# Kernel optimization log

Hardware: AMD Instinct MI355X
Metric: run time of the kernel (lower is better)

Reference implementation:

```python
import jax, jax.numpy as jnp
import numpy as np

LAYER_START = 4   # module init arg layer_start
WIN = 2           # module init arg context_window_size
EPS = 1e-8        # clamp in cosine_similarity_torch


def setup_inputs() -> dict:
    key = jax.random.key(0)
    k1, k2 = jax.random.split(key)
    L_all, B, S, D = 13, 8, 512, 768  # BERT-base: embeddings + 12 layers
    hidden_states = jax.random.normal(k1, (L_all, B, S, D), dtype=jnp.float32)
    lengths = jax.random.randint(k2, (B,), S // 2, S + 1)
    attention_mask = (jnp.arange(S)[None, :] < lengths[:, None]).astype(jnp.int32)
    return {"hidden_states": hidden_states, "attention_mask": attention_mask}


def _wk_forward(hidden_states, attention_mask):
    # hidden_states: (L_all, B, S, D) -> keep layers from LAYER_START on
    x = jnp.transpose(hidden_states, (1, 0, 2, 3))[:, LAYER_START:]  # (B, L, S, D)
    B, L, S, D = x.shape
    feats = jnp.transpose(x, (0, 2, 1, 3))  # (B, S, L, D) per-token layer features

    # ---- unify_token: per-token, QR over windowed layer embeddings ----
    aligns, novs = [], []
    for k in range(L):  # small fixed loop over layers (9 iters)
        left = list(range(k - WIN, k)) if k >= WIN else []
        right = list(range(k + 1, min(k + WIN + 1, L)))
        idx = np.array(left + right + [k])
        n = idx.size  # = window_matrix.size(0) in torch
        A = jnp.swapaxes(feats[:, :, idx, :], -1, -2)  # (B, S, D, n) = window_matrix.T
        _, R = jnp.linalg.qr(A)                        # R: (B, S, n, n)
        r = R[..., :, -1]                              # last column of R
        Rsub = R[..., :-1, :-1]
        # columns of Rsub normalized along dim 0, mean over columns, dot R[:-1,-1]
        Rhat = Rsub / jnp.linalg.norm(Rsub, axis=-2, keepdims=True)
        align = jnp.sum(jnp.mean(Rhat, axis=-1) * R[..., :-1, -1], axis=-1)
        align = align / jnp.linalg.norm(r[..., :-1], axis=-1)
        align = 1.0 / (align * (n * 2))
        nov = jnp.abs(r[..., -1]) / jnp.linalg.norm(r, axis=-1)
        aligns.append(align)
        novs.append(nov)
    align = jnp.stack(aligns, axis=-1)  # (B, S, L)
    nov = jnp.stack(novs, axis=-1)      # (B, S, L)
    align = align / jnp.sum(align, axis=-1, keepdims=True)
    nov = nov / jnp.sum(nov, axis=-1, keepdims=True)
    alpha = align + nov
    alpha = alpha / jnp.sum(alpha, axis=-1, keepdims=True)
    token_emb = jnp.einsum('bsl,bsld->bsd', alpha, feats)  # per-token embedding

    # ---- unify_sentence: variance of sub-diagonal cosine sims across layers ----
    norms = jnp.linalg.norm(feats, axis=-1)  # (B, S, L)
    c = jnp.sum(feats[:, :, 1:] * feats[:, :, :-1], axis=-1)
    c = c / jnp.clip(norms[:, :, 1:] * norms[:, :, :-1], EPS)  # (B, S, L-1)
    var_tok = jnp.var(c, axis=-1, ddof=1)  # torch.var is unbiased

    lengths = jnp.sum(attention_mask, axis=1) - 1  # unmask_num
    valid = jnp.arange(S)[None, :] < lengths[:, None]
    v = jnp.where(valid, var_tok, 0.0)
    v = v / jnp.sum(v, axis=-1, keepdims=True)
    return jnp.einsum('bs,bsd->bd', v, token_emb)  # (B, D)


def reference(hidden_states, attention_mask):
    return _wk_forward(hidden_states, attention_mask)
```

## Files before the change

kernel.cpp:

```cpp
#include <hip/hip_runtime.h>

#define B_ 8
#define S_ 512
#define D_ 768
#define LAYER0 4
#define LSTRIDE4 (8*512*768/4)
#define SCH 32
#define CW (S_/SCH)

__device__ const int QI9[45] = {0,0,0,0,0,0,0,0,0, 1,1,1,1,1,1,1,1, 2,2,2,2,2,2,2,
                                3,3,3,3,3,3, 4,4,4,4,4, 5,5,5,5, 6,6,6, 7,7, 8};
__device__ const int QJ9[45] = {0,1,2,3,4,5,6,7,8, 1,2,3,4,5,6,7,8, 2,3,4,5,6,7,8,
                                3,4,5,6,7,8, 4,5,6,7,8, 5,6,7,8, 6,7,8, 7,8, 8};

__device__ __forceinline__ float dot4(const float4& a, const float4& b) {
  return fmaf(a.x, b.x, fmaf(a.y, b.y, fmaf(a.z, b.z, a.w * b.w)));
}

__global__ __launch_bounds__(64) void wk_token(const float* __restrict__ hid,
                                               const int* __restrict__ mask,
                                               float* __restrict__ wte,
                                               float* __restrict__ wv) {
  const int token = blockIdx.x;
  const int b = token >> 9;
  const int s = token & (S_ - 1);
  const int t = threadIdx.x;

  __shared__ float pgl[64][45];
  __shared__ float Gsym[81];
  __shared__ float st[19];

  const int valid = (s < S_ - 1) ? mask[b * S_ + s + 1] : 0;

  const float4* base = (const float4*)hid
      + (((size_t)LAYER0 * B_ + b) * S_ + s) * (D_ / 4) + t;
  float4 f[27];
#pragma unroll
  for (int l = 0; l < 9; ++l) {
#pragma unroll
    for (int c = 0; c < 3; ++c) f[l * 3 + c] = base[(size_t)l * LSTRIDE4 + c * 64];
  }

  {
    int q = 0;
#pragma unroll
    for (int i = 0; i < 9; ++i) {
#pragma unroll
      for (int j = i; j < 9; ++j) {
        pgl[t][q] = dot4(f[i * 3], f[j * 3])
                  + dot4(f[i * 3 + 1], f[j * 3 + 1])
                  + dot4(f[i * 3 + 2], f[j * 3 + 2]);
        ++q;
      }
    }
  }
  __syncthreads();

  if (t < 45) {
    float a0 = 0.f, a1 = 0.f, a2 = 0.f, a3 = 0.f;
#pragma unroll
    for (int r = 0; r < 64; r += 4) {
      a0 += pgl[r][t]; a1 += pgl[r + 1][t]; a2 += pgl[r + 2][t]; a3 += pgl[r + 3][t];
    }
    float tot = (a0 + a1) + (a2 + a3);
    Gsym[QI9[t] * 9 + QJ9[t]] = tot;
    Gsym[QJ9[t] * 9 + QI9[t]] = tot;
  }
  __syncthreads();

  if (t < 9) {
    const int k = t;
    int nb[4]; int m = 0;
    if (k >= 2) { nb[m++] = k - 2; nb[m++] = k - 1; }
    if (k + 1 < 9) nb[m++] = k + 1;
    if (k + 2 < 9) nb[m++] = k + 2;
    const int n = m + 1;

    float g[4], Lc[4][4], tv[4];
    for (int i = 0; i < m; ++i) g[i] = Gsym[nb[i] * 9 + k];

    for (int i = 0; i < m; ++i) {
      for (int j = 0; j <= i; ++j) {
        float sum = Gsym[nb[i] * 9 + nb[j]];
        for (int p = 0; p < j; ++p) sum -= Lc[i][p] * Lc[j][p];
        Lc[i][j] = (i == j) ? sqrtf(sum) : sum / Lc[j][j];
      }
    }
    float s2 = 0.f;
    for (int i = 0; i < m; ++i) {
      float sum = g[i];
      for (int p = 0; p < i; ++p) sum -= Lc[i][p] * tv[p];
      tv[i] = sum / Lc[i][i];
      s2 += tv[i] * tv[i];
    }
    float ar = 0.f;
    for (int i = 0; i < m; ++i) ar += g[i] / sqrtf(Gsym[nb[i] * 9 + nb[i]]);
    ar /= (float)m;

    st[k] = sqrtf(s2) / (ar * (2.0f * (float)n));
    float Gkk = Gsym[k * 9 + k];
    st[9 + k] = sqrtf(fmaxf(Gkk - s2, 0.f)) / sqrtf(Gkk);
  }
  if (t == 9) {
    float sc = 0.f, sc2 = 0.f;
    for (int i = 0; i < 8; ++i) {
      float nn = sqrtf(Gsym[i * 9 + i]) * sqrtf(Gsym[(i + 1) * 9 + i + 1]);
      nn = fmaxf(nn, 1e-8f);
      float ci = Gsym[i * 9 + i + 1] / nn;
      sc += ci; sc2 += ci * ci;
    }
    float mean = sc * 0.125f;
    st[18] = (sc2 - 8.f * mean * mean) * (1.f / 7.f);
  }
  __syncthreads();

  const float w = valid ? st[18] : 0.f;
  float sa = 0.f, sn = 0.f;
#pragma unroll
  for (int l = 0; l < 9; ++l) { sa += st[l]; sn += st[9 + l]; }
  const float rsa = 1.f / sa, rsn = 1.f / sn;
  float a9[9]; float ss = 0.f;
#pragma unroll
  for (int l = 0; l < 9; ++l) { a9[l] = st[l] * rsa + st[9 + l] * rsn; ss += a9[l]; }
  const float inv = w / ss;

  float4* o = (float4*)wte + (size_t)token * (D_ / 4) + t;
#pragma unroll
  for (int c = 0; c < 3; ++c) {
    float4 acc = make_float4(0.f, 0.f, 0.f, 0.f);
#pragma unroll
    for (int l = 0; l < 9; ++l) {
      float a = a9[l] * inv;
      float4 p = f[l * 3 + c];
      acc.x += a * p.x; acc.y += a * p.y; acc.z += a * p.z; acc.w += a * p.w;
    }
    o[c * 64] = acc;
  }
  if (t == 0) wv[token] = w;
}

__global__ __launch_bounds__(192) void wk_pool(const float* __restrict__ wte,
                                               const float* __restrict__ wv,
                                               float* __restrict__ P,
                                               float* __restrict__ Pw) {
  const int b = blockIdx.x >> 5;
  const int c = blockIdx.x & 31;
  const int t = threadIdx.x;

  float4 a = make_float4(0.f, 0.f, 0.f, 0.f);
  const float4* base = (const float4*)wte + ((size_t)b * S_ + c * CW) * (D_ / 4) + t;
#pragma unroll 4
  for (int sl = 0; sl < CW; ++sl) {
    float4 p = base[sl * (D_ / 4)];
    a.x += p.x; a.y += p.y; a.z += p.z; a.w += p.w;
  }
  ((float4*)P)[(size_t)blockIdx.x * (D_ / 4) + t] = a;
  if (t == 0) {
    float ws = 0.f;
#pragma unroll
    for (int i = 0; i < CW; ++i) ws += wv[b * S_ + c * CW + i];
    Pw[blockIdx.x] = ws;
  }
}

__global__ __launch_bounds__(256) void wk_pool_final(const float* __restrict__ P,
                                                     const float* __restrict__ Pw,
                                                     float* __restrict__ out) {
  const int i = blockIdx.x * 256 + threadIdx.x;
  const int b = i / (D_ / 4);
  const int d4 = i % (D_ / 4);
  float n0 = 0.f, n1 = 0.f, n2 = 0.f, n3 = 0.f, den = 0.f;
#pragma unroll
  for (int c = 0; c < SCH; ++c) {
    float4 p = ((const float4*)P)[((size_t)b * SCH + c) * (D_ / 4) + d4];
    n0 += p.x; n1 += p.y; n2 += p.z; n3 += p.w;
    den += Pw[b * SCH + c];
  }
  float inv = 1.f / den;
  ((float4*)out)[i] = make_float4(n0 * inv, n1 * inv, n2 * inv, n3 * inv);
}

extern "C" void kernel_launch(void* const* d_in, const int* in_sizes, int n_in,
                              void* d_out, int out_size, void* d_ws, size_t ws_size,
                              hipStream_t stream) {
  const float* hid = (const float*)d_in[0];
  const int* mask = (const int*)d_in[1];
  float* out = (float*)d_out;

  float* wte = (float*)d_ws;
  float* wv  = wte + (size_t)B_ * S_ * D_;
  float* P   = wv + B_ * S_;
  float* Pw  = P + (size_t)B_ * SCH * D_;

  wk_token<<<B_ * S_, 64, 0, stream>>>(hid, mask, wte, wv);
  wk_pool<<<B_ * SCH, 192, 0, stream>>>(wte, wv, P, Pw);
  wk_pool_final<<<(B_ * (D_ / 4) + 255) / 256, 256, 0, stream>>>(P, Pw, out);
}
```

Before: 52.29 us.

## Emit per-token layer weights and re-read hidden states in the pooling kernel

The token kernel no longer keeps all nine layers of features in registers. It streams one 256-float chunk at a time into Gram partials and reduces them with wave shuffles before a smaller LDS stage. Instead of writing a 768-wide weighted token embedding, it writes nine per-token layer weights. The pooling kernel then re-reads the nine hidden-state layers and applies those weights itself. This removes the intermediate embedding write and read and lowers register pressure, but the large hidden-state tensor is read twice, and the second read happens in a kernel with only 256 blocks.

```diff
diff --git a/kernel.cpp b/kernel.cpp
--- a/kernel.cpp
+++ b/kernel.cpp
@@ -17,16 +17,15 @@
   return fmaf(a.x, b.x, fmaf(a.y, b.y, fmaf(a.z, b.z, a.w * b.w)));
 }
 
-__global__ __launch_bounds__(64) void wk_token(const float* __restrict__ hid,
-                                               const int* __restrict__ mask,
-                                               float* __restrict__ wte,
-                                               float* __restrict__ wv) {
+__global__ __launch_bounds__(64, 4) void wk_token(const float* __restrict__ hid,
+                                                  const int* __restrict__ mask,
+                                                  float* __restrict__ wa) {
   const int token = blockIdx.x;
   const int b = token >> 9;
   const int s = token & (S_ - 1);
   const int t = threadIdx.x;
 
-  __shared__ float pgl[64][45];
+  __shared__ float pgl[16][45];
   __shared__ float Gsym[81];
   __shared__ float st[19];
 
@@ -34,35 +33,43 @@
 
   const float4* base = (const float4*)hid
       + (((size_t)LAYER0 * B_ + b) * S_ + s) * (D_ / 4) + t;
-  float4 f[27];
-#pragma unroll
-  for (int l = 0; l < 9; ++l) {
-#pragma unroll
-    for (int c = 0; c < 3; ++c) f[l * 3 + c] = base[(size_t)l * LSTRIDE4 + c * 64];
-  }
-
-  {
+  float pp[45];
+#pragma unroll
+  for (int q = 0; q < 45; ++q) pp[q] = 0.f;
+
+#pragma unroll
+  for (int c = 0; c < 3; ++c) {
+    float4 g[9];
+#pragma unroll
+    for (int l = 0; l < 9; ++l) g[l] = base[(size_t)l * LSTRIDE4 + c * 64];
     int q = 0;
 #pragma unroll
     for (int i = 0; i < 9; ++i) {
 #pragma unroll
       for (int j = i; j < 9; ++j) {
-        pgl[t][q] = dot4(f[i * 3], f[j * 3])
-                  + dot4(f[i * 3 + 1], f[j * 3 + 1])
-                  + dot4(f[i * 3 + 2], f[j * 3 + 2]);
+        pp[q] += dot4(g[i], g[j]);
         ++q;
       }
     }
   }
+
+#pragma unroll
+  for (int q = 0; q < 45; ++q) {
+    pp[q] += __shfl_xor(pp[q], 1);
+    pp[q] += __shfl_xor(pp[q], 2);
+  }
+  if ((t & 3) == 0) {
+    const int r = t >> 2;
+#pragma unroll
+    for (int q = 0; q < 45; ++q) pgl[r][q] = pp[q];
+  }
   __syncthreads();
 
   if (t < 45) {
-    float a0 = 0.f, a1 = 0.f, a2 = 0.f, a3 = 0.f;
-#pragma unroll
-    for (int r = 0; r < 64; r += 4) {
-      a0 += pgl[r][t]; a1 += pgl[r + 1][t]; a2 += pgl[r + 2][t]; a3 += pgl[r + 3][t];
-    }
-    float tot = (a0 + a1) + (a2 + a3);
+    float a0 = 0.f, a1 = 0.f;
+#pragma unroll
+    for (int r = 0; r < 16; r += 2) { a0 += pgl[r][t]; a1 += pgl[r + 1][t]; }
+    float tot = a0 + a1;
     Gsym[QI9[t] * 9 + QJ9[t]] = tot;
     Gsym[QJ9[t] * 9 + QI9[t]] = tot;
   }
@@ -114,51 +121,51 @@
   }
   __syncthreads();
 
-  const float w = valid ? st[18] : 0.f;
-  float sa = 0.f, sn = 0.f;
-#pragma unroll
-  for (int l = 0; l < 9; ++l) { sa += st[l]; sn += st[9 + l]; }
-  const float rsa = 1.f / sa, rsn = 1.f / sn;
-  float a9[9]; float ss = 0.f;
-#pragma unroll
-  for (int l = 0; l < 9; ++l) { a9[l] = st[l] * rsa + st[9 + l] * rsn; ss += a9[l]; }
-  const float inv = w / ss;
-
-  float4* o = (float4*)wte + (size_t)token * (D_ / 4) + t;
-#pragma unroll
-  for (int c = 0; c < 3; ++c) {
-    float4 acc = make_float4(0.f, 0.f, 0.f, 0.f);
-#pragma unroll
-    for (int l = 0; l < 9; ++l) {
-      float a = a9[l] * inv;
-      float4 p = f[l * 3 + c];
-      acc.x += a * p.x; acc.y += a * p.y; acc.z += a * p.z; acc.w += a * p.w;
-    }
-    o[c * 64] = acc;
-  }
-  if (t == 0) wv[token] = w;
-}
-
-__global__ __launch_bounds__(192) void wk_pool(const float* __restrict__ wte,
-                                               const float* __restrict__ wv,
+  if (t < 9) {
+    float sa = 0.f, sn = 0.f;
+#pragma unroll
+    for (int l = 0; l < 9; ++l) { sa += st[l]; sn += st[9 + l]; }
+    const float rsa = 1.f / sa, rsn = 1.f / sn;
+    float ss = 0.f;
+#pragma unroll
+    for (int l = 0; l < 9; ++l) ss += st[l] * rsa + st[9 + l] * rsn;
+    const float w = valid ? st[18] : 0.f;
+    const float al = st[t] * rsa + st[9 + t] * rsn;
+    wa[token * 9 + t] = al * (w / ss);
+  }
+}
+
+__global__ __launch_bounds__(192) void wk_pool(const float* __restrict__ hid,
+                                               const float* __restrict__ wa,
                                                float* __restrict__ P,
                                                float* __restrict__ Pw) {
   const int b = blockIdx.x >> 5;
   const int c = blockIdx.x & 31;
   const int t = threadIdx.x;
 
+  __shared__ float ca[CW][9];
+  if (t < CW * 9) ((float*)ca)[t] = wa[((size_t)b * S_ + c * CW) * 9 + t];
+  __syncthreads();
+
   float4 a = make_float4(0.f, 0.f, 0.f, 0.f);
-  const float4* base = (const float4*)wte + ((size_t)b * S_ + c * CW) * (D_ / 4) + t;
+  const float4* base = (const float4*)hid
+      + (((size_t)LAYER0 * B_ + b) * S_ + c * CW) * (D_ / 4) + t;
+#pragma unroll
+  for (int l = 0; l < 9; ++l) {
 #pragma unroll 4
-  for (int sl = 0; sl < CW; ++sl) {
-    float4 p = base[sl * (D_ / 4)];
-    a.x += p.x; a.y += p.y; a.z += p.z; a.w += p.w;
+    for (int sl = 0; sl < CW; ++sl) {
+      float wgt = ca[sl][l];
+      float4 p = base[(size_t)l * LSTRIDE4 + sl * (D_ / 4)];
+      a.x += wgt * p.x; a.y += wgt * p.y; a.z += wgt * p.z; a.w += wgt * p.w;
+    }
   }
   ((float4*)P)[(size_t)blockIdx.x * (D_ / 4) + t] = a;
   if (t == 0) {
     float ws = 0.f;
 #pragma unroll
-    for (int i = 0; i < CW; ++i) ws += wv[b * S_ + c * CW + i];
+    for (int sl = 0; sl < CW; ++sl)
+#pragma unroll
+      for (int l = 0; l < 9; ++l) ws += ca[sl][l];
     Pw[blockIdx.x] = ws;
   }
 }
@@ -187,12 +194,11 @@
   const int* mask = (const int*)d_in[1];
   float* out = (float*)d_out;
 
-  float* wte = (float*)d_ws;
-  float* wv  = wte + (size_t)B_ * S_ * D_;
-  float* P   = wv + B_ * S_;
-  float* Pw  = P + (size_t)B_ * SCH * D_;
-
-  wk_token<<<B_ * S_, 64, 0, stream>>>(hid, mask, wte, wv);
-  wk_pool<<<B_ * SCH, 192, 0, stream>>>(wte, wv, P, Pw);
+  float* wa = (float*)d_ws;
+  float* P  = wa + (size_t)B_ * S_ * 9;
+  float* Pw = P + (size_t)B_ * SCH * D_;
+
+  wk_token<<<B_ * S_, 64, 0, stream>>>(hid, mask, wa);
+  wk_pool<<<B_ * SCH, 192, 0, stream>>>(hid, wa, P, Pw);
   wk_pool_final<<<(B_ * (D_ / 4) + 255) / 256, 256, 0, stream>>>(P, Pw, out);
 }
```

After: 131.3 us. 2.51x slower.

## Fuse token weighting with partial pooling in 4-token blocks, drop intermediate buffer

Applied to the files above, without the earlier changes.

Each block now handles four tokens, one per wavefront, and sums their weighted token embeddings in shared memory before writing one partial row per block. This removes the full per-token embedding write and the separate pooling kernel that read it back, leaving one lighter final reduction kernel. The cost is larger shared memory per block, extra block-wide barriers across the four wavefronts, and a longer final reduction over 128 partials per batch.

```diff
diff --git a/kernel.cpp b/kernel.cpp
--- a/kernel.cpp
+++ b/kernel.cpp
@@ -3,10 +3,10 @@
 #define B_ 8
 #define S_ 512
 #define D_ 768
+#define D4 (D_/4)
 #define LAYER0 4
 #define LSTRIDE4 (8*512*768/4)
-#define SCH 32
-#define CW (S_/SCH)
+#define CPB 128
 
 __device__ const int QI9[45] = {0,0,0,0,0,0,0,0,0, 1,1,1,1,1,1,1,1, 2,2,2,2,2,2,2,
                                 3,3,3,3,3,3, 4,4,4,4,4, 5,5,5,5, 6,6,6, 7,7, 8};
@@ -17,23 +17,25 @@
   return fmaf(a.x, b.x, fmaf(a.y, b.y, fmaf(a.z, b.z, a.w * b.w)));
 }
 
-__global__ __launch_bounds__(64) void wk_token(const float* __restrict__ hid,
-                                               const int* __restrict__ mask,
-                                               float* __restrict__ wte,
-                                               float* __restrict__ wv) {
-  const int token = blockIdx.x;
-  const int b = token >> 9;
-  const int s = token & (S_ - 1);
-  const int t = threadIdx.x;
+__global__ __launch_bounds__(256, 3) void wk_main(const float* __restrict__ hid,
+                                                  const int* __restrict__ mask,
+                                                  float* __restrict__ P,
+                                                  float* __restrict__ Pw) {
+  const int blk = blockIdx.x;
+  const int wid = threadIdx.x >> 6;
+  const int lane = threadIdx.x & 63;
+  const int token = blk * 4 + wid;
+  const int b = token >> 9, s = token & (S_ - 1);
 
-  __shared__ float pgl[64][45];
-  __shared__ float Gsym[81];
-  __shared__ float st[19];
+  __shared__ float pgl[4][64][45];
+  __shared__ float Gsym[4][81];
+  __shared__ float st[4][19];
+  __shared__ float wl[4];
 
   const int valid = (s < S_ - 1) ? mask[b * S_ + s + 1] : 0;
 
   const float4* base = (const float4*)hid
-      + (((size_t)LAYER0 * B_ + b) * S_ + s) * (D_ / 4) + t;
+      + (((size_t)LAYER0 * B_ + b) * S_ + s) * D4 + lane;
   float4 f[27];
 #pragma unroll
   for (int l = 0; l < 9; ++l) {
@@ -47,29 +49,30 @@
     for (int i = 0; i < 9; ++i) {
 #pragma unroll
       for (int j = i; j < 9; ++j) {
-        pgl[t][q] = dot4(f[i * 3], f[j * 3])
-                  + dot4(f[i * 3 + 1], f[j * 3 + 1])
-                  + dot4(f[i * 3 + 2], f[j * 3 + 2]);
+        pgl[wid][lane][q] = dot4(f[i * 3], f[j * 3])
+                          + dot4(f[i * 3 + 1], f[j * 3 + 1])
+                          + dot4(f[i * 3 + 2], f[j * 3 + 2]);
         ++q;
       }
     }
   }
   __syncthreads();
 
-  if (t < 45) {
+  if (lane < 45) {
     float a0 = 0.f, a1 = 0.f, a2 = 0.f, a3 = 0.f;
 #pragma unroll
     for (int r = 0; r < 64; r += 4) {
-      a0 += pgl[r][t]; a1 += pgl[r + 1][t]; a2 += pgl[r + 2][t]; a3 += pgl[r + 3][t];
+      a0 += pgl[wid][r][lane];     a1 += pgl[wid][r + 1][lane];
+      a2 += pgl[wid][r + 2][lane]; a3 += pgl[wid][r + 3][lane];
     }
     float tot = (a0 + a1) + (a2 + a3);
-    Gsym[QI9[t] * 9 + QJ9[t]] = tot;
-    Gsym[QJ9[t] * 9 + QI9[t]] = tot;
+    Gsym[wid][QI9[lane] * 9 + QJ9[lane]] = tot;
+    Gsym[wid][QJ9[lane] * 9 + QI9[lane]] = tot;
   }
   __syncthreads();
 
-  if (t < 9) {
-    const int k = t;
+  if (lane < 9) {
+    const int k = lane;
     int nb[4]; int m = 0;
     if (k >= 2) { nb[m++] = k - 2; nb[m++] = k - 1; }
     if (k + 1 < 9) nb[m++] = k + 1;
@@ -77,11 +80,11 @@
     const int n = m + 1;
 
     float g[4], Lc[4][4], tv[4];
-    for (int i = 0; i < m; ++i) g[i] = Gsym[nb[i] * 9 + k];
+    for (int i = 0; i < m; ++i) g[i] = Gsym[wid][nb[i] * 9 + k];
 
     for (int i = 0; i < m; ++i) {
       for (int j = 0; j <= i; ++j) {
-        float sum = Gsym[nb[i] * 9 + nb[j]];
+        float sum = Gsym[wid][nb[i] * 9 + nb[j]];
         for (int p = 0; p < j; ++p) sum -= Lc[i][p] * Lc[j][p];
         Lc[i][j] = (i == j) ? sqrtf(sum) : sum / Lc[j][j];
       }
@@ -94,90 +97,85 @@
       s2 += tv[i] * tv[i];
     }
     float ar = 0.f;
-    for (int i = 0; i < m; ++i) ar += g[i] / sqrtf(Gsym[nb[i] * 9 + nb[i]]);
+    for (int i = 0; i < m; ++i) ar += g[i] / sqrtf(Gsym[wid][nb[i] * 9 + nb[i]]);
     ar /= (float)m;
 
-    st[k] = sqrtf(s2) / (ar * (2.0f * (float)n));
-    float Gkk = Gsym[k * 9 + k];
-    st[9 + k] = sqrtf(fmaxf(Gkk - s2, 0.f)) / sqrtf(Gkk);
+    st[wid][k] = sqrtf(s2) / (ar * (2.0f * (float)n));
+    float Gkk = Gsym[wid][k * 9 + k];
+    st[wid][9 + k] = sqrtf(fmaxf(Gkk - s2, 0.f)) / sqrtf(Gkk);
   }
-  if (t == 9) {
+  if (lane == 9) {
     float sc = 0.f, sc2 = 0.f;
     for (int i = 0; i < 8; ++i) {
-      float nn = sqrtf(Gsym[i * 9 + i]) * sqrtf(Gsym[(i + 1) * 9 + i + 1]);
+      float nn = sqrtf(Gsym[wid][i * 9 + i]) * sqrtf(Gsym[wid][(i + 1) * 9 + i + 1]);
       nn = fmaxf(nn, 1e-8f);
-      float ci = Gsym[i * 9 + i + 1] / nn;
+      float ci = Gsym[wid][i * 9 + i + 1] / nn;
       sc += ci; sc2 += ci * ci;
     }
     float mean = sc * 0.125f;
-    st[18] = (sc2 - 8.f * mean * mean) * (1.f / 7.f);
+    st[wid][18] = (sc2 - 8.f * mean * mean) * (1.f / 7.f);
   }
   __syncthreads();
 
-  const float w = valid ? st[18] : 0.f;
+  const float w = valid ? st[wid][18] : 0.f;
   float sa = 0.f, sn = 0.f;
 #pragma unroll
-  for (int l = 0; l < 9; ++l) { sa += st[l]; sn += st[9 + l]; }
+  for (int l = 0; l < 9; ++l) { sa += st[wid][l]; sn += st[wid][9 + l]; }
   const float rsa = 1.f / sa, rsn = 1.f / sn;
   float a9[9]; float ss = 0.f;
 #pragma unroll
-  for (int l = 0; l < 9; ++l) { a9[l] = st[l] * rsa + st[9 + l] * rsn; ss += a9[l]; }
+  for (int l = 0; l < 9; ++l) { a9[l] = st[wid][l] * rsa + st[wid][9 + l] * rsn; ss += a9[l]; }
   const float inv = w / ss;
 
-  float4* o = (float4*)wte + (size_t)token * (D_ / 4) + t;
+  float4 acc0 = {0,0,0,0}, acc1 = {0,0,0,0}, acc2 = {0,0,0,0};
 #pragma unroll
-  for (int c = 0; c < 3; ++c) {
-    float4 acc = make_float4(0.f, 0.f, 0.f, 0.f);
-#pragma unroll
-    for (int l = 0; l < 9; ++l) {
-      float a = a9[l] * inv;
-      float4 p = f[l * 3 + c];
-      acc.x += a * p.x; acc.y += a * p.y; acc.z += a * p.z; acc.w += a * p.w;
-    }
-    o[c * 64] = acc;
+  for (int l = 0; l < 9; ++l) {
+    const float a = a9[l] * inv;
+    acc0.x += a * f[l*3].x;   acc0.y += a * f[l*3].y;   acc0.z += a * f[l*3].z;   acc0.w += a * f[l*3].w;
+    acc1.x += a * f[l*3+1].x; acc1.y += a * f[l*3+1].y; acc1.z += a * f[l*3+1].z; acc1.w += a * f[l*3+1].w;
+    acc2.x += a * f[l*3+2].x; acc2.y += a * f[l*3+2].y; acc2.z += a * f[l*3+2].z; acc2.w += a * f[l*3+2].w;
   }
-  if (t == 0) wv[token] = w;
+
+  float4* teacc = (float4*)&pgl[0][0][0];
+  teacc[wid * D4 + 0 * 64 + lane] = acc0;
+  teacc[wid * D4 + 1 * 64 + lane] = acc1;
+  teacc[wid * D4 + 2 * 64 + lane] = acc2;
+  if (lane == 0) wl[wid] = w;
+  __syncthreads();
+
+  const int i = threadIdx.x;
+  if (i < D4) {
+    float4 r0 = teacc[i], r1 = teacc[D4 + i], r2 = teacc[2 * D4 + i], r3 = teacc[3 * D4 + i];
+    float4 rr = make_float4((r0.x + r1.x) + (r2.x + r3.x),
+                            (r0.y + r1.y) + (r2.y + r3.y),
+                            (r0.z + r1.z) + (r2.z + r3.z),
+                            (r0.w + r1.w) + (r2.w + r3.w));
+    ((float4*)P)[(size_t)blk * D4 + i] = rr;
+  }
+  if (i == 192) Pw[blk] = (wl[0] + wl[1]) + (wl[2] + wl[3]);
 }
 
-__global__ __launch_bounds__(192) void wk_pool(const float* __restrict__ wte,
-                                               const float* __restrict__ wv,
-                                               float* __restrict__ P,
-                                               float* __restrict__ Pw) {
-  const int b = blockIdx.x >> 5;
-  const int c = blockIdx.x & 31;
-  const int t = threadIdx.x;
+__global__ __launch_bounds__(64) void wk_final(const float* __restrict__ P,
+                                               const float* __restrict__ Pw,
+                                               float* __restrict__ out) {
+  const int blk = blockIdx.x;
+  const int b = blk / 3;
+  const int i = (blk % 3) * 64 + threadIdx.x;
 
-  float4 a = make_float4(0.f, 0.f, 0.f, 0.f);
-  const float4* base = (const float4*)wte + ((size_t)b * S_ + c * CW) * (D_ / 4) + t;
-#pragma unroll 4
-  for (int sl = 0; sl < CW; ++sl) {
-    float4 p = base[sl * (D_ / 4)];
-    a.x += p.x; a.y += p.y; a.z += p.z; a.w += p.w;
+  float d0 = 0.f, d1 = 0.f;
+#pragma unroll 8
+  for (int c = 0; c < CPB; c += 2) { d0 += Pw[b * CPB + c]; d1 += Pw[b * CPB + c + 1]; }
+  const float den = d0 + d1;
+
+  float4 n = {0.f, 0.f, 0.f, 0.f};
+  const float4* p = (const float4*)P + (size_t)b * CPB * D4 + i;
+#pragma unroll 8
+  for (int c = 0; c < CPB; ++c) {
+    float4 v = p[(size_t)c * D4];
+    n.x += v.x; n.y += v.y; n.z += v.z; n.w += v.w;
   }
-  ((float4*)P)[(size_t)blockIdx.x * (D_ / 4) + t] = a;
-  if (t == 0) {
-    float ws = 0.f;
-#pragma unroll
-    for (int i = 0; i < CW; ++i) ws += wv[b * S_ + c * CW + i];
-    Pw[blockIdx.x] = ws;
-  }
-}
-
-__global__ __launch_bounds__(256) void wk_pool_final(const float* __restrict__ P,
-                                                     const float* __restrict__ Pw,
-                                                     float* __restrict__ out) {
-  const int i = blockIdx.x * 256 + threadIdx.x;
-  const int b = i / (D_ / 4);
-  const int d4 = i % (D_ / 4);
-  float n0 = 0.f, n1 = 0.f, n2 = 0.f, n3 = 0.f, den = 0.f;
-#pragma unroll
-  for (int c = 0; c < SCH; ++c) {
-    float4 p = ((const float4*)P)[((size_t)b * SCH + c) * (D_ / 4) + d4];
-    n0 += p.x; n1 += p.y; n2 += p.z; n3 += p.w;
-    den += Pw[b * SCH + c];
-  }
-  float inv = 1.f / den;
-  ((float4*)out)[i] = make_float4(n0 * inv, n1 * inv, n2 * inv, n3 * inv);
+  const float r = 1.f / den;
+  ((float4*)out)[b * D4 + i] = make_float4(n.x * r, n.y * r, n.z * r, n.w * r);
 }
 
 extern "C" void kernel_launch(void* const* d_in, const int* in_sizes, int n_in,
@@ -187,12 +185,9 @@
   const int* mask = (const int*)d_in[1];
   float* out = (float*)d_out;
 
-  float* wte = (float*)d_ws;
-  float* wv  = wte + (size_t)B_ * S_ * D_;
-  float* P   = wv + B_ * S_;
-  float* Pw  = P + (size_t)B_ * SCH * D_;
+  float* P  = (float*)d_ws;
+  float* Pw = P + (size_t)B_ * CPB * D_;
 
-  wk_token<<<B_ * S_, 64, 0, stream>>>(hid, mask, wte, wv);
-  wk_pool<<<B_ * SCH, 192, 0, stream>>>(wte, wv, P, Pw);
-  wk_pool_final<<<(B_ * (D_ / 4) + 255) / 256, 256, 0, stream>>>(P, Pw, out);
+  wk_main<<<B_ * CPB, 256, 0, stream>>>(hid, mask, P, Pw);
+  wk_final<<<B_ * 3, 64, 0, stream>>>(P, Pw, out);
 }
```

After: 112.7 us. +115.5%, slower.

## Spread each token's features over 192 threads with quad shuffle reduction

Applied to the files above, without the earlier changes.

The per-token kernel now runs 192 threads per block, each holding one float4 per layer instead of three. This cuts per-thread register use from 27 float4 to 9 and raises occupancy and memory-level parallelism. Partial Gram products are pre-reduced across groups of 4 lanes with xor shuffles, so the shared partial table shrinks to 48 rows. The cost is 45 extra shuffle pairs per thread and a larger block, which adds more sync overhead per token.

```diff
diff --git a/kernel.cpp b/kernel.cpp
--- a/kernel.cpp
+++ b/kernel.cpp
@@ -3,6 +3,7 @@
 #define B_ 8
 #define S_ 512
 #define D_ 768
+#define D4 (D_/4)
 #define LAYER0 4
 #define LSTRIDE4 (8*512*768/4)
 #define SCH 32
@@ -17,29 +18,26 @@
   return fmaf(a.x, b.x, fmaf(a.y, b.y, fmaf(a.z, b.z, a.w * b.w)));
 }
 
-__global__ __launch_bounds__(64) void wk_token(const float* __restrict__ hid,
-                                               const int* __restrict__ mask,
-                                               float* __restrict__ wte,
-                                               float* __restrict__ wv) {
+__global__ __launch_bounds__(192) void wk_token(const float* __restrict__ hid,
+                                                const int* __restrict__ mask,
+                                                float* __restrict__ wte,
+                                                float* __restrict__ wv) {
   const int token = blockIdx.x;
   const int b = token >> 9;
   const int s = token & (S_ - 1);
   const int t = threadIdx.x;
 
-  __shared__ float pgl[64][45];
+  __shared__ float pgl[48][45];
   __shared__ float Gsym[81];
   __shared__ float st[19];
 
   const int valid = (s < S_ - 1) ? mask[b * S_ + s + 1] : 0;
 
   const float4* base = (const float4*)hid
-      + (((size_t)LAYER0 * B_ + b) * S_ + s) * (D_ / 4) + t;
-  float4 f[27];
+      + (((size_t)LAYER0 * B_ + b) * S_ + s) * D4 + t;
+  float4 f[9];
 #pragma unroll
-  for (int l = 0; l < 9; ++l) {
-#pragma unroll
-    for (int c = 0; c < 3; ++c) f[l * 3 + c] = base[(size_t)l * LSTRIDE4 + c * 64];
-  }
+  for (int l = 0; l < 9; ++l) f[l] = base[(size_t)l * LSTRIDE4];
 
   {
     int q = 0;
@@ -47,9 +45,10 @@
     for (int i = 0; i < 9; ++i) {
 #pragma unroll
       for (int j = i; j < 9; ++j) {
-        pgl[t][q] = dot4(f[i * 3], f[j * 3])
-                  + dot4(f[i * 3 + 1], f[j * 3 + 1])
-                  + dot4(f[i * 3 + 2], f[j * 3 + 2]);
+        float v = dot4(f[i], f[j]);
+        v += __shfl_xor(v, 1);
+        v += __shfl_xor(v, 2);
+        if ((t & 3) == 0) pgl[t >> 2][q] = v;
         ++q;
       }
     }
@@ -59,8 +58,9 @@
   if (t < 45) {
     float a0 = 0.f, a1 = 0.f, a2 = 0.f, a3 = 0.f;
 #pragma unroll
-    for (int r = 0; r < 64; r += 4) {
-      a0 += pgl[r][t]; a1 += pgl[r + 1][t]; a2 += pgl[r + 2][t]; a3 += pgl[r + 3][t];
+    for (int r = 0; r < 48; r += 4) {
+      a0 += pgl[r][t];     a1 += pgl[r + 1][t];
+      a2 += pgl[r + 2][t]; a3 += pgl[r + 3][t];
     }
     float tot = (a0 + a1) + (a2 + a3);
     Gsym[QI9[t] * 9 + QJ9[t]] = tot;
@@ -124,18 +124,13 @@
   for (int l = 0; l < 9; ++l) { a9[l] = st[l] * rsa + st[9 + l] * rsn; ss += a9[l]; }
   const float inv = w / ss;
 
-  float4* o = (float4*)wte + (size_t)token * (D_ / 4) + t;
+  float4 acc = {0.f, 0.f, 0.f, 0.f};
 #pragma unroll
-  for (int c = 0; c < 3; ++c) {
-    float4 acc = make_float4(0.f, 0.f, 0.f, 0.f);
-#pragma unroll
-    for (int l = 0; l < 9; ++l) {
-      float a = a9[l] * inv;
-      float4 p = f[l * 3 + c];
-      acc.x += a * p.x; acc.y += a * p.y; acc.z += a * p.z; acc.w += a * p.w;
-    }
-    o[c * 64] = acc;
+  for (int l = 0; l < 9; ++l) {
+    const float a = a9[l] * inv;
+    acc.x += a * f[l].x; acc.y += a * f[l].y; acc.z += a * f[l].z; acc.w += a * f[l].w;
   }
+  ((float4*)wte)[(size_t)token * D4 + t] = acc;
   if (t == 0) wv[token] = w;
 }
 
@@ -148,13 +143,13 @@
   const int t = threadIdx.x;
 
   float4 a = make_float4(0.f, 0.f, 0.f, 0.f);
-  const float4* base = (const float4*)wte + ((size_t)b * S_ + c * CW) * (D_ / 4) + t;
+  const float4* base = (const float4*)wte + ((size_t)b * S_ + c * CW) * D4 + t;
 #pragma unroll 4
   for (int sl = 0; sl < CW; ++sl) {
-    float4 p = base[sl * (D_ / 4)];
+    float4 p = base[sl * D4];
     a.x += p.x; a.y += p.y; a.z += p.z; a.w += p.w;
   }
-  ((float4*)P)[(size_t)blockIdx.x * (D_ / 4) + t] = a;
+  ((float4*)P)[(size_t)blockIdx.x * D4 + t] = a;
   if (t == 0) {
     float ws = 0.f;
 #pragma unroll
@@ -167,12 +162,12 @@
                                                      const float* __restrict__ Pw,
                                                      float* __restrict__ out) {
   const int i = blockIdx.x * 256 + threadIdx.x;
-  const int b = i / (D_ / 4);
-  const int d4 = i % (D_ / 4);
+  const int b = i / D4;
+  const int d4 = i % D4;
   float n0 = 0.f, n1 = 0.f, n2 = 0.f, n3 = 0.f, den = 0.f;
 #pragma unroll
   for (int c = 0; c < SCH; ++c) {
-    float4 p = ((const float4*)P)[((size_t)b * SCH + c) * (D_ / 4) + d4];
+    float4 p = ((const float4*)P)[((size_t)b * SCH + c) * D4 + d4];
     n0 += p.x; n1 += p.y; n2 += p.z; n3 += p.w;
     den += Pw[b * SCH + c];
   }
@@ -192,7 +187,7 @@
   float* P   = wv + B_ * S_;
   float* Pw  = P + (size_t)B_ * SCH * D_;
 
-  wk_token<<<B_ * S_, 64, 0, stream>>>(hid, mask, wte, wv);
+  wk_token<<<B_ * S_, 192, 0, stream>>>(hid, mask, wte, wv);
   wk_pool<<<B_ * SCH, 192, 0, stream>>>(wte, wv, P, Pw);
-  wk_pool_final<<<(B_ * (D_ / 4) + 255) / 256, 256, 0, stream>>>(P, Pw, out);
+  wk_pool_final<<<(B_ * D4 + 255) / 256, 256, 0, stream>>>(P, Pw, out);
 }
```

New measurement: 61.55 us. 17.7% more time.
